# Kernel tuning notes

Hardware: AMD Instinct MI355X
Metric: run time of the kernel (lower is better)

## Reference

```python
import jax, jax.numpy as jnp
import numpy as np

ALPHA = 0.65
KERNEL_RADIUS = 3
BIG = 1e30  # stand-in for +inf in morphological (tropical) convolution


def morphological_kernel(finsler_params, kernel_radius, alpha):
    """Sample the fractional morphological kernel on a (2r+1)x(2r+1) grid.

    F_c(x,y) = sqrt(x^2+y^2) * exp(-sum_k params[c,k] * B_k(theta)) with
    B_1=cos(t), B_2=sin(t), B_3=cos(2t), ... (circular harmonics).
    Kernel for the alpha-homogeneous HJB PDE (t=1):
      k(x) = nu_a * F(x)^(2a/(2a-1)),  nu_a = (2a-1)*(2a)^(-2a/(2a-1)).
    """
    r = kernel_radius
    coords = jnp.arange(-r, r + 1, dtype=finsler_params.dtype)
    yy = coords[:, None]  # [kh,1]
    xx = coords[None, :]  # [1,kw]
    rho = jnp.sqrt(xx * xx + yy * yy)              # [kh,kw]
    theta = jnp.arctan2(yy + 0 * xx, xx + 0 * yy)  # [kh,kw]
    K = finsler_params.shape[1]
    ks = np.arange(1, K + 1)
    freqs = jnp.asarray((ks + 1) // 2, dtype=finsler_params.dtype)  # 1,1,2,2,...
    ang = freqs[:, None, None] * theta[None]                        # [K,kh,kw]
    is_cos = jnp.asarray(ks % 2 == 1)[:, None, None]
    basis = jnp.where(is_cos, jnp.cos(ang), jnp.sin(ang))           # [K,kh,kw]
    F = rho[None] * jnp.exp(-jnp.einsum('ck,kij->cij', finsler_params, basis))  # [C,kh,kw]
    p = 2.0 * alpha / (2.0 * alpha - 1.0)
    nu = (2.0 * alpha - 1.0) * (2.0 * alpha) ** (-p)
    return nu * F ** p  # zero at origin since p>0


def morphological_convolution(u, kernel):
    """out[b,c,y,x] = min_{dy,dx} u[b,c,y+dy,x+dx] + kernel[c,dy+r,dx+r].
    Scan over the (2r+1)^2 stencil offsets with a running min (no huge patches)."""
    B, C, H, W = u.shape
    kh, kw = kernel.shape[1], kernel.shape[2]
    r = kh // 2
    pad = jnp.pad(u, ((0, 0), (0, 0), (r, r), (r, r)), constant_values=BIG)
    kflat = kernel.reshape(C, kh * kw)
    dys, dxs = jnp.meshgrid(jnp.arange(kh), jnp.arange(kw), indexing='ij')
    offs = jnp.stack([dys.reshape(-1), dxs.reshape(-1)], axis=-1)  # [kh*kw,2]

    def step(carry, i):
        dy, dx = offs[i, 0], offs[i, 1]
        sl = jax.lax.dynamic_slice(pad, (0, 0, dy, dx), (B, C, H, W))
        cand = sl + kflat[:, i][None, :, None, None]
        return jnp.minimum(carry, cand), None

    init = jnp.full((B, C, H, W), BIG, u.dtype)
    out, _ = jax.lax.scan(step, init, jnp.arange(kh * kw))
    return out


def convection(u, c):
    """Translation-equivariant transport: out(x) = u(x - c_channel), bilinear
    interpolation, replicate boundary. c[:,0]=x-shift, c[:,1]=y-shift."""
    B, C, H, W = u.shape
    gy = jnp.arange(H, dtype=u.dtype)[None, :, None] - c[:, 1][:, None, None]  # [C,H,1]
    gx = jnp.arange(W, dtype=u.dtype)[None, None, :] - c[:, 0][:, None, None]  # [C,1,W]
    y0 = jnp.floor(gy)
    x0 = jnp.floor(gx)
    wy = gy - y0  # [C,H,1]
    wx = gx - x0  # [C,1,W]
    y0i = jnp.clip(y0.astype(jnp.int32), 0, H - 1)
    y1i = jnp.clip(y0i + 1, 0, H - 1)
    x0i = jnp.clip(x0.astype(jnp.int32), 0, W - 1)
    x1i = jnp.clip(x0i + 1, 0, W - 1)
    ci = jnp.arange(C)[:, None, None]

    def gather(yi, xi):  # yi:[C,H,1], xi:[C,1,W] -> [B,C,H,W]
        return u[:, ci, yi, xi]

    return ((1 - wy) * (1 - wx) * gather(y0i, x0i)
            + (1 - wy) * wx * gather(y0i, x1i)
            + wy * (1 - wx) * gather(y1i, x0i)
            + wy * wx * gather(y1i, x1i))


def cde_pde_layer(x, c, finsler_dil, finsler_ero, weight):
    u = convection(x, c)
    k_dil = morphological_kernel(finsler_dil, KERNEL_RADIUS, ALPHA)
    u = -morphological_convolution(-u, k_dil)           # fractional dilation
    k_ero = morphological_kernel(finsler_ero, KERNEL_RADIUS, ALPHA)
    u = morphological_convolution(u, k_ero)             # fractional erosion
    return jnp.einsum('bihw,io->bohw', u, weight)       # linear channel mix


def setup_inputs() -> dict:
    key = jax.random.key(0)
    k1, k2, k3, k4, k5 = jax.random.split(key, 5)
    B, Cin, Cout, H, W, K = 16, 32, 32, 256, 256, 4
    x = jax.random.normal(k1, (B, Cin, H, W), dtype=jnp.float32)
    c = jax.random.normal(k2, (Cin, 2), dtype=jnp.float32)  # ~kaiming-uniform scale
    finsler_dil = jax.random.uniform(k3, (Cin, K), minval=-1.0, maxval=1.0, dtype=jnp.float32)
    finsler_ero = jax.random.uniform(k4, (Cin, K), minval=-1.0, maxval=1.0, dtype=jnp.float32)
    weight = jax.random.normal(k5, (Cin, Cout), dtype=jnp.float32) / np.sqrt(Cin)
    return {"x": x, "c": c, "finsler_dil": finsler_dil, "finsler_ero": finsler_ero, "weight": weight}


def reference(x, c, finsler_dil, finsler_ero, weight):
    return cde_pde_layer(x, c, finsler_dil, finsler_ero, weight)
```

## Files before the change

### kernel.cpp

```cpp
#include <hip/hip_runtime.h>
#include <math.h>

#define HH 256
#define WW 256
#define NB 16
#define NC 32
#define RAD 3
#define KWID 7
#define NTAPS 49
#define TILE 64
#define CW 76
#define CH 76
#define BUFSZ (CH * CW + 8)
#define BIGF 1e30f
#define FLT_MAX_C 3.402823466e+38f

__global__ void kgen_kernel(const float* __restrict__ fd,
                            const float* __restrict__ fe,
                            float* __restrict__ kd,
                            float* __restrict__ ke) {
    const int c = blockIdx.x;
    const int t = threadIdx.x;
    if (t >= NTAPS) return;
    const int dy = t / KWID - RAD;
    const int dx = t % KWID - RAD;
    const double rho = sqrt((double)(dx * dx + dy * dy));
    const double th  = atan2((double)dy, (double)dx);
    const double alpha = 0.65;
    const double p  = 2.0 * alpha / (2.0 * alpha - 1.0);
    const double nu = (2.0 * alpha - 1.0) * pow(2.0 * alpha, -p);
    const double b1 = cos(th), b2 = sin(th), b3 = cos(2.0 * th), b4 = sin(2.0 * th);
    double s, F;
    s = (double)fd[c * 4 + 0] * b1 + (double)fd[c * 4 + 1] * b2
      + (double)fd[c * 4 + 2] * b3 + (double)fd[c * 4 + 3] * b4;
    F = rho * exp(-s);
    kd[c * NTAPS + t] = (float)(nu * pow(F, p));
    s = (double)fe[c * 4 + 0] * b1 + (double)fe[c * 4 + 1] * b2
      + (double)fe[c * 4 + 2] * b3 + (double)fe[c * 4 + 3] * b4;
    F = rho * exp(-s);
    ke[c * NTAPS + t] = (float)(nu * pow(F, p));
}

__global__ __launch_bounds__(256, 6) void cde_stencil_kernel(
    const float* __restrict__ xin, const float* __restrict__ csh,
    const float* __restrict__ kdil, const float* __restrict__ kero,
    float* __restrict__ uout)
{
    __shared__ float buf[BUFSZ];

    const int tid = threadIdx.x;
    const int tileId = blockIdx.x;
    const int c = blockIdx.y;
    const int b = blockIdx.z;
    const int ty0 = (tileId >> 2) * TILE;
    const int tx0 = (tileId & 3) * TILE;

    const float cx = csh[c * 2 + 0];
    const float cy = csh[c * 2 + 1];
    const float* __restrict__ xb = xin + (((size_t)b * NC + c) << 16);

    const float mcx = -cx, mcy = -cy;
    const float fx0 = floorf(mcx), fy0 = floorf(mcy);
    const float wxf = mcx - fx0, wyf = mcy - fy0;
    const int IX = (int)fx0, IY = (int)fy0;
    const float w00 = (1.f - wyf) * (1.f - wxf);
    const float w01 = (1.f - wyf) * wxf;
    const float w10 = wyf * (1.f - wxf);
    const float w11 = wyf * wxf;

    {
        int row = tid / CW;
        int col = tid - row * CW;
        for (int idx = tid; idx < CH * CW; idx += 256) {
            const int gy = ty0 - 6 + row;
            const int gx = tx0 - 6 + col;
            float v = -BIGF;
            if (gy >= 0 && gy < HH && gx >= 0 && gx < WW) {
                const int y0 = min(max(gy + IY, 0), HH - 1);
                const int y1 = min(y0 + 1, HH - 1);
                const int x0 = min(max(gx + IX, 0), WW - 1);
                const int x1 = min(x0 + 1, WW - 1);
                const float a00 = xb[(y0 << 8) + x0];
                const float a01 = xb[(y0 << 8) + x1];
                const float a10 = xb[(y1 << 8) + x0];
                const float a11 = xb[(y1 << 8) + x1];
                v = w00 * a00 + w01 * a01 + w10 * a10 + w11 * a11;
            }
            buf[idx] = v;
            col += 28; row += 3;
            if (col >= CW) { col -= CW; ++row; }
        }
    }
    __syncthreads();

    float acc2[5][4];
    int dc0 = 0, dr0 = 0;
    const bool act2 = (tid < 252);
    {
        const float* __restrict__ kdc = kdil + c * NTAPS;
        float ta[NTAPS];
        #pragma unroll
        for (int t = 0; t < NTAPS; ++t) ta[t] = kdc[t];

        if (act2) {
            dc0 = (tid % 18) * 4;
            dr0 = (tid / 18) * 5;

            #pragma unroll
            for (int i = 0; i < 5; ++i)
                #pragma unroll
                for (int j = 0; j < 4; ++j) acc2[i][j] = -FLT_MAX_C;

            const int rb = dr0 * CW + dc0;
            #pragma unroll
            for (int rr = 0; rr < 11; ++rr) {
                const float* rp = &buf[rb + rr * CW];
                const float4 L0 = *reinterpret_cast<const float4*>(rp);
                const float4 L1 = *reinterpret_cast<const float4*>(rp + 4);
                const float2 L2 = *reinterpret_cast<const float2*>(rp + 8);
                const float ld[10] = {L0.x, L0.y, L0.z, L0.w,
                                      L1.x, L1.y, L1.z, L1.w, L2.x, L2.y};
                #pragma unroll
                for (int i = 0; i < 5; ++i) {
                    const int ky = rr - i;
                    if (ky < 0 || ky > 6) continue;
                    const int kb = ky * KWID;
                    #pragma unroll
                    for (int j = 0; j < 4; ++j) {
                        float m = acc2[i][j];
                        m = fmaxf(m, fmaxf(ld[j + 0] - ta[kb + 0], ld[j + 1] - ta[kb + 1]));
                        m = fmaxf(m, fmaxf(ld[j + 2] - ta[kb + 2], ld[j + 3] - ta[kb + 3]));
                        m = fmaxf(m, fmaxf(ld[j + 4] - ta[kb + 4], ld[j + 5] - ta[kb + 5]));
                        m = fmaxf(m, ld[j + 6] - ta[kb + 6]);
                        acc2[i][j] = m;
                    }
                }
            }
        }
    }
    __syncthreads();

    if (act2) {
        #pragma unroll
        for (int i = 0; i < 5; ++i) {
            const int dr = dr0 + i;
            const int gy = ty0 - 3 + dr;
            const bool rOK = (gy >= 0) && (gy < HH);
            const int gxb = tx0 - 3 + dc0;
            float4 st;
            st.x = (rOK && (gxb + 0) >= 0 && (gxb + 0) < WW) ? acc2[i][0] : BIGF;
            st.y = (rOK && (gxb + 1) >= 0 && (gxb + 1) < WW) ? acc2[i][1] : BIGF;
            st.z = (rOK && (gxb + 2) >= 0 && (gxb + 2) < WW) ? acc2[i][2] : BIGF;
            st.w = (rOK && (gxb + 3) >= 0 && (gxb + 3) < WW) ? acc2[i][3] : BIGF;
            *reinterpret_cast<float4*>(&buf[dr * CW + dc0]) = st;
        }
    }
    __syncthreads();

    {
        const float* __restrict__ kec = kero + c * NTAPS;
        float te[NTAPS];
        #pragma unroll
        for (int t = 0; t < NTAPS; ++t) te[t] = kec[t];

        const int ec0 = (tid & 15) * 4;
        const int er0 = (tid >> 4) * 4;

        float acc[4][4];
        #pragma unroll
        for (int i = 0; i < 4; ++i)
            #pragma unroll
            for (int j = 0; j < 4; ++j) acc[i][j] = FLT_MAX_C;

        const int rb = er0 * CW + ec0;
        #pragma unroll
        for (int rr = 0; rr < 10; ++rr) {
            const float* rp = &buf[rb + rr * CW];
            const float4 L0 = *reinterpret_cast<const float4*>(rp);
            const float4 L1 = *reinterpret_cast<const float4*>(rp + 4);
            const float2 L2 = *reinterpret_cast<const float2*>(rp + 8);
            const float ld[10] = {L0.x, L0.y, L0.z, L0.w,
                                  L1.x, L1.y, L1.z, L1.w, L2.x, L2.y};
            #pragma unroll
            for (int i = 0; i < 4; ++i) {
                const int ky = rr - i;
                if (ky < 0 || ky > 6) continue;
                const int kb = ky * KWID;
                #pragma unroll
                for (int j = 0; j < 4; ++j) {
                    float m = acc[i][j];
                    m = fminf(m, fminf(ld[j + 0] + te[kb + 0], ld[j + 1] + te[kb + 1]));
                    m = fminf(m, fminf(ld[j + 2] + te[kb + 2], ld[j + 3] + te[kb + 3]));
                    m = fminf(m, fminf(ld[j + 4] + te[kb + 4], ld[j + 5] + te[kb + 5]));
                    m = fminf(m, ld[j + 6] + te[kb + 6]);
                    acc[i][j] = m;
                }
            }
        }

        float* __restrict__ ob = uout + (((size_t)b * NC + c) << 16);
        #pragma unroll
        for (int i = 0; i < 4; ++i) {
            float4 st;
            st.x = acc[i][0]; st.y = acc[i][1]; st.z = acc[i][2]; st.w = acc[i][3];
            *reinterpret_cast<float4*>(&ob[((ty0 + er0 + i) << 8) + tx0 + ec0]) = st;
        }
    }
}

#define PXS 128
__global__ __launch_bounds__(256) void mix_kernel(float* __restrict__ u,
                                                  const float* __restrict__ wmat) {
    __shared__ float s[NC * PXS];

    const int tid = threadIdx.x;
    const int strip = blockIdx.x;
    const int b = blockIdx.y;
    float* __restrict__ ub = u + ((size_t)b << 21) + strip * PXS;

    #pragma unroll
    for (int k = 0; k < 4; ++k) {
        const int idx = tid + k * 256;
        const int i = idx >> 5;
        const int q = idx & 31;
        const float4 v = *reinterpret_cast<const float4*>(ub + (i << 16) + (q << 2));
        *reinterpret_cast<float4*>(&s[idx << 2]) = v;
    }
    __syncthreads();

    const int lane = tid & 63;
    const int wv = __builtin_amdgcn_readfirstlane(tid) >> 6;
    const int o0 = wv * 8;

    float2 acc[8];
    #pragma unroll
    for (int o = 0; o < 8; ++o) { acc[o].x = 0.f; acc[o].y = 0.f; }

    #pragma unroll
    for (int i = 0; i < NC; ++i) {
        const float2 v = *reinterpret_cast<const float2*>(&s[i * PXS + 2 * lane]);
        const float* __restrict__ wr = wmat + i * NC + o0;
        #pragma unroll
        for (int o = 0; o < 8; ++o) {
            const float w = wr[o];
            acc[o].x = fmaf(v.x, w, acc[o].x);
            acc[o].y = fmaf(v.y, w, acc[o].y);
        }
    }

    #pragma unroll
    for (int o = 0; o < 8; ++o) {
        *reinterpret_cast<float2*>(ub + ((size_t)(o0 + o) << 16) + 2 * lane) = acc[o];
    }
}

extern "C" void kernel_launch(void* const* d_in, const int* in_sizes, int n_in,
                              void* d_out, int out_size, void* d_ws, size_t ws_size,
                              hipStream_t stream) {
    const float* x  = (const float*)d_in[0];
    const float* c  = (const float*)d_in[1];
    const float* fd = (const float*)d_in[2];
    const float* fe = (const float*)d_in[3];
    const float* w  = (const float*)d_in[4];
    float* out = (float*)d_out;

    float* kd = (float*)d_ws;
    float* ke = kd + NC * NTAPS;

    kgen_kernel<<<dim3(NC), dim3(64), 0, stream>>>(fd, fe, kd, ke);
    cde_stencil_kernel<<<dim3(16, NC, NB), dim3(256), 0, stream>>>(x, c, kd, ke, out);
    mix_kernel<<<dim3((HH * WW) / PXS, NB), dim3(256), 0, stream>>>(out, w);
}
```

Before: 455.4 us.

## Run dilation/erosion stencil in packed fp16 with halved shared buffer

Converts the shift-interpolated tile and the intermediate dilation result to fp16 in shared memory. Both min-plus stencils now use packed half2 add and max/min, with alignbit building the odd-offset pairs, and kernel taps are precomputed as duplicated fp16 pairs. The aim is to roughly halve the ALU instruction count and the shared-memory footprint, allowing more resident blocks (launch bound raised to 8). The trade is fp16 rounding of activations and kernel values, plus taps clamped to 57344, which may exceed the correctness tolerance.

Result: faster. 426.5 us (-6.3%).

```diff
diff --git a/kernel.cpp b/kernel.cpp
--- a/kernel.cpp
+++ b/kernel.cpp
@@ -11,14 +11,25 @@
 #define TILE 64
 #define CW 76
 #define CH 76
-#define BUFSZ (CH * CW + 8)
+#define BUFH (CH * CW + 16)
 #define BIGF 1e30f
-#define FLT_MAX_C 3.402823466e+38f
+#define PADF  -57344.0f
+#define TAPCLAMP 57344.0f
+#define HBB 0x7B80u
+
+typedef _Float16 h2 __attribute__((ext_vector_type(2)));
+
+static __device__ __forceinline__ h2 h2_u(unsigned int u) {
+    union { unsigned int u; h2 h; } cv; cv.u = u; return cv.h;
+}
+static __device__ __forceinline__ unsigned int u_h2(h2 h) {
+    union { unsigned int u; h2 h; } cv; cv.h = h; return cv.u;
+}
 
 __global__ void kgen_kernel(const float* __restrict__ fd,
                             const float* __restrict__ fe,
-                            float* __restrict__ kd,
-                            float* __restrict__ ke) {
+                            unsigned int* __restrict__ kd,
+                            unsigned int* __restrict__ ke) {
     const int c = blockIdx.x;
     const int t = threadIdx.x;
     if (t >= NTAPS) return;
@@ -34,19 +45,27 @@
     s = (double)fd[c * 4 + 0] * b1 + (double)fd[c * 4 + 1] * b2
       + (double)fd[c * 4 + 2] * b3 + (double)fd[c * 4 + 3] * b4;
     F = rho * exp(-s);
-    kd[c * NTAPS + t] = (float)(nu * pow(F, p));
+    {
+        const float kv = fminf((float)(nu * pow(F, p)), TAPCLAMP);
+        union { _Float16 h; unsigned short u; } cv; cv.h = (_Float16)(-kv);
+        kd[c * NTAPS + t] = (unsigned int)cv.u | ((unsigned int)cv.u << 16);
+    }
     s = (double)fe[c * 4 + 0] * b1 + (double)fe[c * 4 + 1] * b2
       + (double)fe[c * 4 + 2] * b3 + (double)fe[c * 4 + 3] * b4;
     F = rho * exp(-s);
-    ke[c * NTAPS + t] = (float)(nu * pow(F, p));
-}
-
-__global__ __launch_bounds__(256, 6) void cde_stencil_kernel(
+    {
+        const float kv = fminf((float)(nu * pow(F, p)), TAPCLAMP);
+        union { _Float16 h; unsigned short u; } cv; cv.h = (_Float16)(kv);
+        ke[c * NTAPS + t] = (unsigned int)cv.u | ((unsigned int)cv.u << 16);
+    }
+}
+
+__global__ __launch_bounds__(256, 8) void cde_stencil_kernel(
     const float* __restrict__ xin, const float* __restrict__ csh,
-    const float* __restrict__ kdil, const float* __restrict__ kero,
+    const unsigned int* __restrict__ kdil, const unsigned int* __restrict__ kero,
     float* __restrict__ uout)
 {
-    __shared__ float buf[BUFSZ];
+    __shared__ __align__(16) _Float16 bufh[BUFH];
 
     const int tid = threadIdx.x;
     const int tileId = blockIdx.x;
@@ -74,7 +93,7 @@
         for (int idx = tid; idx < CH * CW; idx += 256) {
             const int gy = ty0 - 6 + row;
             const int gx = tx0 - 6 + col;
-            float v = -BIGF;
+            float v = PADF;
             if (gy >= 0 && gy < HH && gx >= 0 && gx < WW) {
                 const int y0 = min(max(gy + IY, 0), HH - 1);
                 const int y1 = min(y0 + 1, HH - 1);
@@ -86,19 +105,19 @@
                 const float a11 = xb[(y1 << 8) + x1];
                 v = w00 * a00 + w01 * a01 + w10 * a10 + w11 * a11;
             }
-            buf[idx] = v;
+            bufh[idx] = (_Float16)v;
             col += 28; row += 3;
             if (col >= CW) { col -= CW; ++row; }
         }
     }
     __syncthreads();
 
-    float acc2[5][4];
+    h2 acc2[5][2];
     int dc0 = 0, dr0 = 0;
     const bool act2 = (tid < 252);
     {
-        const float* __restrict__ kdc = kdil + c * NTAPS;
-        float ta[NTAPS];
+        const unsigned int* __restrict__ kdc = kdil + c * NTAPS;
+        unsigned int ta[NTAPS];
         #pragma unroll
         for (int t = 0; t < NTAPS; ++t) ta[t] = kdc[t];
 
@@ -106,34 +125,40 @@
             dc0 = (tid % 18) * 4;
             dr0 = (tid / 18) * 5;
 
+            const _Float16 NINF = (_Float16)(-65504.0f);
             #pragma unroll
-            for (int i = 0; i < 5; ++i)
-                #pragma unroll
-                for (int j = 0; j < 4; ++j) acc2[i][j] = -FLT_MAX_C;
+            for (int i = 0; i < 5; ++i) {
+                acc2[i][0] = (h2){NINF, NINF};
+                acc2[i][1] = (h2){NINF, NINF};
+            }
 
             const int rb = dr0 * CW + dc0;
             #pragma unroll
             for (int rr = 0; rr < 11; ++rr) {
-                const float* rp = &buf[rb + rr * CW];
-                const float4 L0 = *reinterpret_cast<const float4*>(rp);
-                const float4 L1 = *reinterpret_cast<const float4*>(rp + 4);
-                const float2 L2 = *reinterpret_cast<const float2*>(rp + 8);
-                const float ld[10] = {L0.x, L0.y, L0.z, L0.w,
-                                      L1.x, L1.y, L1.z, L1.w, L2.x, L2.y};
+                const int base = rb + rr * CW;
+                const uint2 A = *reinterpret_cast<const uint2*>(&bufh[base]);
+                const uint2 B = *reinterpret_cast<const uint2*>(&bufh[base + 4]);
+                const unsigned int w4 = *reinterpret_cast<const unsigned int*>(&bufh[base + 8]);
+                const unsigned int w[5] = {A.x, A.y, B.x, B.y, w4};
+                unsigned int sh[4];
+                #pragma unroll
+                for (int j = 0; j < 4; ++j)
+                    sh[j] = __builtin_amdgcn_alignbit(w[j + 1], w[j], 16);
+                const unsigned int seq0[7] = {w[0], sh[0], w[1], sh[1], w[2], sh[2], w[3]};
+                const unsigned int seq1[7] = {w[1], sh[1], w[2], sh[2], w[3], sh[3], w[4]};
                 #pragma unroll
                 for (int i = 0; i < 5; ++i) {
                     const int ky = rr - i;
                     if (ky < 0 || ky > 6) continue;
                     const int kb = ky * KWID;
+                    h2 a0 = acc2[i][0], a1 = acc2[i][1];
                     #pragma unroll
-                    for (int j = 0; j < 4; ++j) {
-                        float m = acc2[i][j];
-                        m = fmaxf(m, fmaxf(ld[j + 0] - ta[kb + 0], ld[j + 1] - ta[kb + 1]));
-                        m = fmaxf(m, fmaxf(ld[j + 2] - ta[kb + 2], ld[j + 3] - ta[kb + 3]));
-                        m = fmaxf(m, fmaxf(ld[j + 4] - ta[kb + 4], ld[j + 5] - ta[kb + 5]));
-                        m = fmaxf(m, ld[j + 6] - ta[kb + 6]);
-                        acc2[i][j] = m;
+                    for (int kx = 0; kx < 7; ++kx) {
+                        const h2 k2 = h2_u(ta[kb + kx]);
+                        a0 = __builtin_elementwise_max(a0, h2_u(seq0[kx]) + k2);
+                        a1 = __builtin_elementwise_max(a1, h2_u(seq1[kx]) + k2);
                     }
+                    acc2[i][0] = a0; acc2[i][1] = a1;
                 }
             }
         }
@@ -141,60 +166,68 @@
     __syncthreads();
 
     if (act2) {
+        const int gxb = tx0 - 3 + dc0;
         #pragma unroll
         for (int i = 0; i < 5; ++i) {
             const int dr = dr0 + i;
             const int gy = ty0 - 3 + dr;
             const bool rOK = (gy >= 0) && (gy < HH);
-            const int gxb = tx0 - 3 + dc0;
-            float4 st;
-            st.x = (rOK && (gxb + 0) >= 0 && (gxb + 0) < WW) ? acc2[i][0] : BIGF;
-            st.y = (rOK && (gxb + 1) >= 0 && (gxb + 1) < WW) ? acc2[i][1] : BIGF;
-            st.z = (rOK && (gxb + 2) >= 0 && (gxb + 2) < WW) ? acc2[i][2] : BIGF;
-            st.w = (rOK && (gxb + 3) >= 0 && (gxb + 3) < WW) ? acc2[i][3] : BIGF;
-            *reinterpret_cast<float4*>(&buf[dr * CW + dc0]) = st;
+            unsigned int m0 = u_h2(acc2[i][0]);
+            unsigned int m1 = u_h2(acc2[i][1]);
+            if (!(rOK && gxb + 0 >= 0 && gxb + 0 < WW)) m0 = (m0 & 0xFFFF0000u) | HBB;
+            if (!(rOK && gxb + 1 >= 0 && gxb + 1 < WW)) m0 = (m0 & 0x0000FFFFu) | (HBB << 16);
+            if (!(rOK && gxb + 2 >= 0 && gxb + 2 < WW)) m1 = (m1 & 0xFFFF0000u) | HBB;
+            if (!(rOK && gxb + 3 >= 0 && gxb + 3 < WW)) m1 = (m1 & 0x0000FFFFu) | (HBB << 16);
+            uint2 st; st.x = m0; st.y = m1;
+            *reinterpret_cast<uint2*>(&bufh[dr * CW + dc0]) = st;
         }
     }
     __syncthreads();
 
     {
-        const float* __restrict__ kec = kero + c * NTAPS;
-        float te[NTAPS];
+        const unsigned int* __restrict__ kec = kero + c * NTAPS;
+        unsigned int te[NTAPS];
         #pragma unroll
         for (int t = 0; t < NTAPS; ++t) te[t] = kec[t];
 
         const int ec0 = (tid & 15) * 4;
         const int er0 = (tid >> 4) * 4;
 
-        float acc[4][4];
-        #pragma unroll
-        for (int i = 0; i < 4; ++i)
+        h2 acc[4][2];
+        const _Float16 PINF = (_Float16)(65504.0f);
+        #pragma unroll
+        for (int i = 0; i < 4; ++i) {
+            acc[i][0] = (h2){PINF, PINF};
+            acc[i][1] = (h2){PINF, PINF};
+        }
+
+        const int rb = er0 * CW + ec0;
+        #pragma unroll
+        for (int rr = 0; rr < 10; ++rr) {
+            const int base = rb + rr * CW;
+            const uint2 A = *reinterpret_cast<const uint2*>(&bufh[base]);
+            const uint2 B = *reinterpret_cast<const uint2*>(&bufh[base + 4]);
+            const unsigned int w4 = *reinterpret_cast<const unsigned int*>(&bufh[base + 8]);
+            const unsigned int w[5] = {A.x, A.y, B.x, B.y, w4};
+            unsigned int sh[4];
             #pragma unroll
-            for (int j = 0; j < 4; ++j) acc[i][j] = FLT_MAX_C;
-
-        const int rb = er0 * CW + ec0;
-        #pragma unroll
-        for (int rr = 0; rr < 10; ++rr) {
-            const float* rp = &buf[rb + rr * CW];
-            const float4 L0 = *reinterpret_cast<const float4*>(rp);
-            const float4 L1 = *reinterpret_cast<const float4*>(rp + 4);
-            const float2 L2 = *reinterpret_cast<const float2*>(rp + 8);
-            const float ld[10] = {L0.x, L0.y, L0.z, L0.w,
-                                  L1.x, L1.y, L1.z, L1.w, L2.x, L2.y};
+            for (int j = 0; j < 4; ++j)
+                sh[j] = __builtin_amdgcn_alignbit(w[j + 1], w[j], 16);
+            const unsigned int seq0[7] = {w[0], sh[0], w[1], sh[1], w[2], sh[2], w[3]};
+            const unsigned int seq1[7] = {w[1], sh[1], w[2], sh[2], w[3], sh[3], w[4]};
             #pragma unroll
             for (int i = 0; i < 4; ++i) {
                 const int ky = rr - i;
                 if (ky < 0 || ky > 6) continue;
                 const int kb = ky * KWID;
+                h2 a0 = acc[i][0], a1 = acc[i][1];
                 #pragma unroll
-                for (int j = 0; j < 4; ++j) {
-                    float m = acc[i][j];
-                    m = fminf(m, fminf(ld[j + 0] + te[kb + 0], ld[j + 1] + te[kb + 1]));
-                    m = fminf(m, fminf(ld[j + 2] + te[kb + 2], ld[j + 3] + te[kb + 3]));
-                    m = fminf(m, fminf(ld[j + 4] + te[kb + 4], ld[j + 5] + te[kb + 5]));
-                    m = fminf(m, ld[j + 6] + te[kb + 6]);
-                    acc[i][j] = m;
+                for (int kx = 0; kx < 7; ++kx) {
+                    const h2 k2 = h2_u(te[kb + kx]);
+                    a0 = __builtin_elementwise_min(a0, h2_u(seq0[kx]) + k2);
+                    a1 = __builtin_elementwise_min(a1, h2_u(seq1[kx]) + k2);
                 }
+                acc[i][0] = a0; acc[i][1] = a1;
             }
         }
 
@@ -202,7 +235,8 @@
         #pragma unroll
         for (int i = 0; i < 4; ++i) {
             float4 st;
-            st.x = acc[i][0]; st.y = acc[i][1]; st.z = acc[i][2]; st.w = acc[i][3];
+            st.x = (float)acc[i][0].x; st.y = (float)acc[i][0].y;
+            st.z = (float)acc[i][1].x; st.w = (float)acc[i][1].y;
             *reinterpret_cast<float4*>(&ob[((ty0 + er0 + i) << 8) + tx0 + ec0]) = st;
         }
     }
@@ -264,8 +298,8 @@
     const float* w  = (const float*)d_in[4];
     float* out = (float*)d_out;
 
-    float* kd = (float*)d_ws;
-    float* ke = kd + NC * NTAPS;
+    unsigned int* kd = (unsigned int*)d_ws;
+    unsigned int* ke = kd + NC * NTAPS;
 
     kgen_kernel<<<dim3(NC), dim3(64), 0, stream>>>(fd, fe, kd, ke);
     cde_stencil_kernel<<<dim3(16, NC, NB), dim3(256), 0, stream>>>(x, c, kd, ke, out);
```
